# Performance work log

Hardware: AMD Instinct MI355X
Metric: run time of the kernel (lower is better)

Reference implementation:

```python
import jax, jax.numpy as jnp
import numpy as np

SEQ, D_IN, D_OUT, RANK, N_ADAPTERS = 8192, 4096, 4096, 16, 8


def setup_inputs() -> dict:
    key = jax.random.key(0)
    ks = jax.random.split(key, 7)
    return {
        "x": jax.random.normal(ks[0], (SEQ, D_IN), jnp.float32),
        "weight": jax.random.normal(ks[1], (D_IN, D_OUT), jnp.float32) * (D_IN ** -0.5),
        "bias": jax.random.normal(ks[2], (D_OUT,), jnp.float32),
        "A_buffer": jax.random.normal(ks[3], (N_ADAPTERS, RANK, D_IN), jnp.float32) * (D_IN ** -0.5),
        "B_buffer": jax.random.normal(ks[4], (N_ADAPTERS, D_OUT, RANK), jnp.float32) * (RANK ** -0.5),
        "scalings": jax.random.uniform(ks[5], (SEQ,), jnp.float32, 0.5, 2.0),
        "token_indices": jax.random.randint(ks[6], (SEQ,), 0, N_ADAPTERS, jnp.int32),
    }


def reference(x, weight, bias, A_buffer, B_buffer, scalings, token_indices):
    # Base linear layer: [S, D_in] @ [D_in, D_out] + bias
    base_output = x @ weight + bias
    n_adapters = A_buffer.shape[0]
    delta = jnp.zeros_like(base_output)
    # Grouped LoRA GEMM: per-adapter small GEMMs, masked scatter back per token.
    for e in range(n_adapters):
        # run_lora_a_gemm: x @ A[e]^T with per-token scaling -> [S, rank]
        a_out = (x @ A_buffer[e].T) * scalings[:, None]
        # run_lora_b_gemm: a_out @ B[e]^T -> [S, D_out]
        b_out = a_out @ B_buffer[e].T
        delta = delta + jnp.where((token_indices == e)[:, None], b_out, 0.0)
    return base_output + delta
```

## Files before the change

### kernel.cpp

```cpp
#include <hip/hip_runtime.h>
#include <hip/hip_bf16.h>
#include <cstdint>

#define SEQ   8192
#define DIN   4096
#define DOUT  4096
#define RANK  16
#define NAD   8
#define KC    (DIN + NAD*RANK)

using f32x4  = __attribute__((ext_vector_type(4))) float;
using bf16x8 = __attribute__((ext_vector_type(8))) short;

__device__ __forceinline__ unsigned short f2bf(float f) {
  union { float f; uint32_t u; } v; v.f = f;
  return (unsigned short)((v.u + 0x7fffu + ((v.u >> 16) & 1u)) >> 16);
}

__device__ __forceinline__ void async_copy16(void* lds, const void* gmem) {
  __builtin_amdgcn_global_load_lds(
      (__attribute__((address_space(1))) void*)(uintptr_t)gmem,
      (__attribute__((address_space(3))) void*)(uint32_t)(uintptr_t)lds,
      16, 0, 0);
}


__global__ void cvt_xa_kernel(const float* __restrict__ x, unsigned short* __restrict__ xcat,
                              const float* __restrict__ a, unsigned short* __restrict__ abf) {
  if (blockIdx.x < 4096) {
    const int64_t nchunks = (int64_t)SEQ * DIN / 8;
    for (int64_t c = (int64_t)blockIdx.x * 256 + threadIdx.x; c < nchunks;
         c += (int64_t)4096 * 256) {
      int64_t base = c * 8;
      int s = (int)(base >> 12);
      int k = (int)(base & (DIN - 1));
      float4 p = *(const float4*)(x + base);
      float4 q = *(const float4*)(x + base + 4);
      union { unsigned short h[8]; int4 v; } o;
      o.h[0]=f2bf(p.x); o.h[1]=f2bf(p.y); o.h[2]=f2bf(p.z); o.h[3]=f2bf(p.w);
      o.h[4]=f2bf(q.x); o.h[5]=f2bf(q.y); o.h[6]=f2bf(q.z); o.h[7]=f2bf(q.w);
      *(int4*)(xcat + (int64_t)s * KC + k) = o.v;
    }
  } else {
    int c = (blockIdx.x - 4096) * 256 + threadIdx.x;
    int64_t base = (int64_t)c * 8;
    float4 p = *(const float4*)(a + base);
    float4 q = *(const float4*)(a + base + 4);
    union { unsigned short h[8]; int4 v; } o;
    o.h[0]=f2bf(p.x); o.h[1]=f2bf(p.y); o.h[2]=f2bf(p.z); o.h[3]=f2bf(p.w);
    o.h[4]=f2bf(q.x); o.h[5]=f2bf(q.y); o.h[6]=f2bf(q.z); o.h[7]=f2bf(q.w);
    *(int4*)(abf + base) = o.v;
  }
}

__global__ void cvt_wb_kernel(const float* __restrict__ w, unsigned short* __restrict__ wcat,
                              const float* __restrict__ Bbuf) {
  if (blockIdx.x < 4096) {
    __shared__ unsigned short tls[64 * 68];
    int tt = threadIdx.x;
    int n0 = (blockIdx.x & 63) * 64;
    int k0 = (blockIdx.x >> 6) * 64;
#pragma unroll
    for (int j = 0; j < 8; j++) {
      int idx = j * 256 + tt;
      int kk = (idx >> 6) * 2;
      int nn = idx & 63;
      unsigned int lo = f2bf(w[(int64_t)(k0 + kk)     * DOUT + n0 + nn]);
      unsigned int hi = f2bf(w[(int64_t)(k0 + kk + 1) * DOUT + n0 + nn]);
      *(unsigned int*)&tls[nn * 68 + kk] = lo | (hi << 16);
    }
    __syncthreads();
#pragma unroll
    for (int pp = 0; pp < 4; pp++) {
      int flat = pp * 256 + tt;
      int nn = flat >> 4;
      int kk4 = (flat & 15) * 4;
      uint2 v = *(const uint2*)&tls[nn * 68 + kk4];
      *(uint2*)(wcat + (int64_t)(n0 + nn) * KC + k0 + kk4) = v;
    }
  } else {
    int idx = (blockIdx.x - 4096) * 256 + threadIdx.x;
    int n = idx >> 7, er = idx & 127;
    int e = er >> 4, r = er & 15;
    float v = Bbuf[((int64_t)e * DOUT + n) * RANK + r];
    wcat[(int64_t)n * KC + DIN + er] = f2bf(v);
  }
}

__global__ __launch_bounds__(512, 2) void gemm_lora_a2(
    const unsigned short* __restrict__ A,
    const unsigned short* __restrict__ Bb,
    const float* __restrict__ scal,
    const int* __restrict__ tok,
    unsigned short* __restrict__ xcat) {
  constexpr int BK = 64;
  __shared__ unsigned short sA[2][32 * BK];
  __shared__ unsigned short sB[2][128 * BK];
  int tid = threadIdx.x, wave = tid >> 6, lane = tid & 63;
  int quad = lane >> 4, l16 = lane & 15;
  int rm = wave >> 2, cn = wave & 3;
  int row0 = blockIdx.x * 32;
  int f8 = l16 & 7;

  f32x4 acc[2];
  acc[0] = f32x4{0.f, 0.f, 0.f, 0.f};
  acc[1] = f32x4{0.f, 0.f, 0.f, 0.f};

  auto stage = [&](int b, int kt) {
    int k0 = kt * BK;
    if (tid < 256) {
      int r = tid >> 3, kc = ((tid & 7) ^ (r & 7)) * 8;
      async_copy16(&sA[b][tid * 8], A + (int64_t)(row0 + r) * KC + k0 + kc);
    }
#pragma unroll
    for (int i = 0; i < 2; i++) {
      int c = i * 512 + tid;
      int r = c >> 3, kc = ((c & 7) ^ (r & 7)) * 8;
      async_copy16(&sB[b][c * 8], Bb + (int64_t)r * DIN + k0 + kc);
    }
  };

  stage(0, 0);
  __syncthreads();

  for (int kt = 0; kt < DIN / BK; ++kt) {
    int cur = kt & 1;
    if (kt + 1 < DIN / BK) stage(cur ^ 1, kt + 1);
    const unsigned short* sAc = sA[cur];
    const unsigned short* sBc = sB[cur];
#pragma unroll
    for (int ks = 0; ks < 2; ks++) {
      int qp = ((ks * 4 + quad) ^ f8) * 8;
      bf16x8 af = *(const bf16x8*)&sAc[(rm * 16 + l16) * BK + qp];
      bf16x8 b0 = *(const bf16x8*)&sBc[(cn * 32 + l16) * BK + qp];
      bf16x8 b1 = *(const bf16x8*)&sBc[(cn * 32 + 16 + l16) * BK + qp];
      acc[0] = __builtin_amdgcn_mfma_f32_16x16x32_bf16(af, b0, acc[0], 0, 0, 0);
      acc[1] = __builtin_amdgcn_mfma_f32_16x16x32_bf16(af, b1, acc[1], 0, 0, 0);
    }
    __syncthreads();
  }

#pragma unroll
  for (int ni = 0; ni < 2; ni++) {
    int er = cn * 32 + ni * 16 + l16;
    int e = er >> 4;
#pragma unroll
    for (int r = 0; r < 4; r++) {
      int s = row0 + rm * 16 + quad * 4 + r;
      float v = acc[ni][r] * scal[s];
      v = (e == tok[s]) ? v : 0.0f;
      xcat[(int64_t)s * KC + DIN + er] = f2bf(v);
    }
  }
}


#define CFENCE asm volatile("" ::: "memory")

template<int MQ>
__device__ __forceinline__ void ldsA(const unsigned short* aT, int wm, int l16, int quad,
                                     bf16x8 (&af)[4][2]) {
  int f8 = l16 & 7;
#pragma unroll
  for (int ks = 0; ks < 2; ks++) {
    int qp = ((ks * 4 + quad) ^ f8) * 8;
#pragma unroll
    for (int mi = 0; mi < 4; mi++)
      af[mi][ks] = *(const bf16x8*)&aT[(wm * 128 + MQ * 64 + mi * 16 + l16) * 64 + qp];
  }
}

template<int NQ>
__device__ __forceinline__ void ldsB(const unsigned short* bT, int wn, int l16, int quad,
                                     bf16x8 (&bq)[2][2]) {
  int f8 = l16 & 7;
#pragma unroll
  for (int ks = 0; ks < 2; ks++) {
    int qp = ((ks * 4 + quad) ^ f8) * 8;
#pragma unroll
    for (int ni = 0; ni < 2; ni++)
      bq[ni][ks] = *(const bf16x8*)&bT[(wn * 64 + NQ * 32 + ni * 16 + l16) * 64 + qp];
  }
}

template<int MQ, int NQ>
__device__ __forceinline__ void mfma_quad(f32x4 (&acc)[8][4], bf16x8 (&af)[4][2],
                                          bf16x8 (&bq)[2][2]) {
  __builtin_amdgcn_s_setprio(1);
#pragma unroll
  for (int mi = 0; mi < 4; mi++)
#pragma unroll
    for (int ni = 0; ni < 2; ni++)
#pragma unroll
      for (int ks = 0; ks < 2; ks++)
        acc[MQ * 4 + mi][NQ * 2 + ni] = __builtin_amdgcn_mfma_f32_16x16x32_bf16(
            af[mi][ks], bq[ni][ks], acc[MQ * 4 + mi][NQ * 2 + ni], 0, 0, 0);
  __builtin_amdgcn_s_setprio(0);
}

__device__ __forceinline__ void stage_A(unsigned short* sAb, const unsigned short* Ag,
                                        int mq, int k0, int tid) {
  int rr  = tid >> 3;
  int q8  = (tid & 7) * 8;
  int qc8 = ((tid & 7) ^ (rr & 7)) * 8;
  int r0 = mq * 64 + rr;
  async_copy16(sAb + r0 * 64 + q8, Ag + (int64_t)r0 * KC + k0 + qc8);
  int r1 = r0 + 128;
  async_copy16(sAb + r1 * 64 + q8, Ag + (int64_t)r1 * KC + k0 + qc8);
}

__device__ __forceinline__ void stage_B(unsigned short* sBb, const unsigned short* Bg,
                                        int nq, int k0, int tid) {
  int rB  = ((tid >> 3) & 31) | ((tid >> 8) << 6);
  int q8  = (tid & 7) * 8;
  int qc8 = ((tid & 7) ^ ((tid >> 3) & 7)) * 8;
  int r0 = nq * 32 + rB;
  async_copy16(sBb + r0 * 64 + q8, Bg + (int64_t)r0 * KC + k0 + qc8);
  int r1 = r0 + 128;
  async_copy16(sBb + r1 * 64 + q8, Bg + (int64_t)r1 * KC + k0 + qc8);
}

#define MIDBAR                                                    \
  CFENCE; __builtin_amdgcn_s_barrier();                           \
  asm volatile("s_waitcnt lgkmcnt(0)" ::: "memory")
#define ENDBAR  CFENCE; __builtin_amdgcn_s_barrier(); CFENCE

#define TILE(aT, bT, S0, S1, S2, S3, BND)                         \
  ldsA<0>(aT, wm, l16, quad, af);                                 \
  ldsB<0>(bT, wn, l16, quad, bf0);                                \
  S0; MIDBAR;                                                     \
  mfma_quad<0, 0>(acc, af, bf0);                                  \
  ENDBAR;                                                         \
  ldsB<1>(bT, wn, l16, quad, bf1);                                \
  S1; MIDBAR;                                                     \
  mfma_quad<0, 1>(acc, af, bf1);                                  \
  ENDBAR;                                                         \
  ldsA<1>(aT, wm, l16, quad, af);                                 \
  S2; MIDBAR;                                                     \
  mfma_quad<1, 1>(acc, af, bf1);                                  \
  ENDBAR;                                                         \
  S3; CFENCE;                                                     \
  mfma_quad<1, 0>(acc, af, bf0);                                  \
  BND;                                                            \
  ENDBAR

__global__ __launch_bounds__(512, 2) void gemm_main8(
    const unsigned short* __restrict__ A,
    const unsigned short* __restrict__ B,
    const float* __restrict__ bias,
    float* __restrict__ out) {
  extern __shared__ unsigned short smem[];
  unsigned short* a0 = smem;
  unsigned short* b0 = smem + 16384;
  unsigned short* a1 = smem + 32768;
  unsigned short* b1 = smem + 49152;

  int tid = threadIdx.x, wave = tid >> 6, lane = tid & 63;
  int quad = lane >> 4, l16 = lane & 15;
  int wm = wave >> 2, wn = wave & 3;

  int bid = blockIdx.x;
  int cid = (bid & 7) * 64 + (bid >> 3);
  int bm = cid >> 4, bn = cid & 15;
  int row0 = bm * 256, col0 = bn * 256;

  const unsigned short* Ag = A + (int64_t)row0 * KC;
  const unsigned short* Bg = B + (int64_t)col0 * KC;

  const f32x4 zero = {0.f, 0.f, 0.f, 0.f};
  f32x4 acc[8][4];
#pragma unroll
  for (int i = 0; i < 8; i++)
#pragma unroll
    for (int j = 0; j < 4; j++) acc[i][j] = zero;

  bf16x8 af[4][2], bf0[2][2], bf1[2][2];

  stage_A(a0, Ag, 0, 0, tid);
  stage_B(b0, Bg, 0, 0, tid);
  stage_B(b0, Bg, 1, 0, tid);
  stage_A(a0, Ag, 1, 0, tid);
  stage_A(a1, Ag, 0, 64, tid);
  stage_B(b1, Bg, 1, 64, tid);
  stage_A(a1, Ag, 1, 64, tid);
  asm volatile("s_waitcnt vmcnt(6)" ::: "memory");
  ENDBAR;

#define BND6 asm volatile("s_waitcnt vmcnt(6)" ::: "memory")

  for (int tp = 0; tp < 32; ++tp) {
    int kE = tp * 128;
    TILE(a0, b0,
         stage_B(b1, Bg, 0, kE + 64,  tid),
         stage_A(a0, Ag, 0, kE + 128, tid),
         stage_B(b0, Bg, 1, kE + 128, tid),
         stage_A(a0, Ag, 1, kE + 128, tid),
         BND6);
    TILE(a1, b1,
         stage_B(b0, Bg, 0, kE + 128, tid),
         stage_A(a1, Ag, 0, kE + 192, tid),
         stage_B(b1, Bg, 1, kE + 192, tid),
         stage_A(a1, Ag, 1, kE + 192, tid),
         BND6);
  }

  TILE(a0, b0,
       stage_B(b1, Bg, 0, 4160, tid),
       (void)0, (void)0, (void)0,
       asm volatile("s_waitcnt vmcnt(0)" ::: "memory"));

  ldsA<0>(a1, wm, l16, quad, af);
  ldsB<0>(b1, wn, l16, quad, bf0);
  mfma_quad<0, 0>(acc, af, bf0);
  ldsB<1>(b1, wn, l16, quad, bf1);
  mfma_quad<0, 1>(acc, af, bf1);
  ldsA<1>(a1, wm, l16, quad, af);
  mfma_quad<1, 1>(acc, af, bf1);
  mfma_quad<1, 0>(acc, af, bf0);

#pragma unroll
  for (int ni = 0; ni < 4; ni++) {
    int col = col0 + wn * 64 + ni * 16 + l16;
    float bv = bias[col];
#pragma unroll
    for (int mi = 0; mi < 8; mi++) {
      int rbase = row0 + wm * 128 + mi * 16 + quad * 4;
#pragma unroll
      for (int r = 0; r < 4; r++)
        out[(int64_t)(rbase + r) * DOUT + col] = acc[mi][ni][r] + bv;
    }
  }
}

__global__ void fb_aout(const float* __restrict__ x, const float* __restrict__ Abuf,
                        const float* __restrict__ scal, const int* __restrict__ tok,
                        float* __restrict__ aout) {
  int s = blockIdx.x;
  int e = tok[s];
  __shared__ float red[256];
  for (int r = 0; r < RANK; ++r) {
    float p = 0.f;
    for (int k = threadIdx.x; k < DIN; k += 256)
      p += x[(int64_t)s * DIN + k] * Abuf[((int64_t)e * RANK + r) * DIN + k];
    red[threadIdx.x] = p;
    __syncthreads();
    for (int off = 128; off > 0; off >>= 1) {
      if (threadIdx.x < off) red[threadIdx.x] += red[threadIdx.x + off];
      __syncthreads();
    }
    if (threadIdx.x == 0) aout[s * RANK + r] = red[0] * scal[s];
    __syncthreads();
  }
}
__global__ void fb_out(const float* __restrict__ x, const float* __restrict__ w,
                       const float* __restrict__ bias, const float* __restrict__ Bbuf,
                       const int* __restrict__ tok, const float* __restrict__ aout,
                       float* __restrict__ out) {
  int64_t idx = (int64_t)blockIdx.x * blockDim.x + threadIdx.x;
  int s = (int)(idx >> 12), n = (int)(idx & (DOUT - 1));
  float accv = bias[n];
  for (int k = 0; k < DIN; ++k)
    accv += x[(int64_t)s * DIN + k] * w[(int64_t)k * DOUT + n];
  int e = tok[s];
  float d = 0.f;
  for (int r = 0; r < RANK; ++r)
    d += aout[s * RANK + r] * Bbuf[((int64_t)e * DOUT + n) * RANK + r];
  out[idx] = accv + d;
}

extern "C" void kernel_launch(void* const* d_in, const int* in_sizes, int n_in,
                              void* d_out, int out_size, void* d_ws, size_t ws_size,
                              hipStream_t stream) {
  const float* x    = (const float*)d_in[0];
  const float* w    = (const float*)d_in[1];
  const float* bias = (const float*)d_in[2];
  const float* Abuf = (const float*)d_in[3];
  const float* Bbuf = (const float*)d_in[4];
  const float* scal = (const float*)d_in[5];
  const int*   tok  = (const int*)d_in[6];
  float* out = (float*)d_out;

  const size_t xcat_b = (size_t)SEQ * KC * 2;
  const size_t wcat_b = (size_t)DOUT * KC * 2;
  const size_t abf_b  = (size_t)NAD * RANK * DIN * 2;

  if (ws_size >= xcat_b + wcat_b + abf_b) {
    static bool lds_attr_done = false;
    if (!lds_attr_done) {
      (void)hipFuncSetAttribute((const void*)gemm_main8,
                                hipFuncAttributeMaxDynamicSharedMemorySize, 131072);
      lds_attr_done = true;
    }
    unsigned short* xcat = (unsigned short*)d_ws;
    unsigned short* wcat = (unsigned short*)((char*)d_ws + xcat_b);
    unsigned short* abf  = (unsigned short*)((char*)d_ws + xcat_b + wcat_b);
    cvt_xa_kernel<<<4352, 256, 0, stream>>>(x, xcat, Abuf, abf);
    cvt_wb_kernel<<<6144, 256, 0, stream>>>(w, wcat, Bbuf);
    gemm_lora_a2<<<256, 512, 0, stream>>>(xcat, abf, scal, tok, xcat);
    gemm_main8<<<512, 512, 131072, stream>>>(xcat, wcat, bias, out);
  } else {
    float* aout = (float*)d_ws;
    fb_aout<<<SEQ, 256, 0, stream>>>(x, Abuf, scal, tok, aout);
    fb_out<<<(int)(((int64_t)SEQ * DOUT) / 256), 256, 0, stream>>>(x, w, bias, Bbuf, tok, aout, out);
  }
}
```

Measured before the change: 552.5 us.

## Fuse x bf16 conversion into LoRA-A GEMM and merge weight/A conversion kernels

The LoRA-A GEMM now reads fp32 x directly, converts each tile to bf16 in registers, writes it into the swizzled LDS tile and also stores it into xcat for the main GEMM. This removes the separate x conversion pass and the re-read of bf16 x from global memory. W/B and A conversions are merged into one launch, saving a kernel launch. In exchange, the LoRA-A kernel uses synchronous global loads for x, which adds register pressure and latency per K step, and it drops the 2-blocks-per-CU launch bound hint. Only 256 blocks now do the x conversion work, so that work is less parallel than before.

```diff
diff --git a/kernel.cpp b/kernel.cpp
--- a/kernel.cpp
+++ b/kernel.cpp
@@ -24,25 +24,40 @@
       16, 0, 0);
 }
 
-
-__global__ void cvt_xa_kernel(const float* __restrict__ x, unsigned short* __restrict__ xcat,
-                              const float* __restrict__ a, unsigned short* __restrict__ abf) {
+__global__ void cvt_wba_kernel(const float* __restrict__ w, unsigned short* __restrict__ wcat,
+                               const float* __restrict__ Bbuf,
+                               const float* __restrict__ a, unsigned short* __restrict__ abf) {
   if (blockIdx.x < 4096) {
-    const int64_t nchunks = (int64_t)SEQ * DIN / 8;
-    for (int64_t c = (int64_t)blockIdx.x * 256 + threadIdx.x; c < nchunks;
-         c += (int64_t)4096 * 256) {
-      int64_t base = c * 8;
-      int s = (int)(base >> 12);
-      int k = (int)(base & (DIN - 1));
-      float4 p = *(const float4*)(x + base);
-      float4 q = *(const float4*)(x + base + 4);
-      union { unsigned short h[8]; int4 v; } o;
-      o.h[0]=f2bf(p.x); o.h[1]=f2bf(p.y); o.h[2]=f2bf(p.z); o.h[3]=f2bf(p.w);
-      o.h[4]=f2bf(q.x); o.h[5]=f2bf(q.y); o.h[6]=f2bf(q.z); o.h[7]=f2bf(q.w);
-      *(int4*)(xcat + (int64_t)s * KC + k) = o.v;
-    }
+    __shared__ unsigned short tls[64 * 68];
+    int tt = threadIdx.x;
+    int n0 = (blockIdx.x & 63) * 64;
+    int k0 = (blockIdx.x >> 6) * 64;
+#pragma unroll
+    for (int j = 0; j < 8; j++) {
+      int idx = j * 256 + tt;
+      int kk = (idx >> 6) * 2;
+      int nn = idx & 63;
+      unsigned int lo = f2bf(w[(int64_t)(k0 + kk)     * DOUT + n0 + nn]);
+      unsigned int hi = f2bf(w[(int64_t)(k0 + kk + 1) * DOUT + n0 + nn]);
+      *(unsigned int*)&tls[nn * 68 + kk] = lo | (hi << 16);
+    }
+    __syncthreads();
+#pragma unroll
+    for (int pp = 0; pp < 4; pp++) {
+      int flat = pp * 256 + tt;
+      int nn = flat >> 4;
+      int kk4 = (flat & 15) * 4;
+      uint2 v = *(const uint2*)&tls[nn * 68 + kk4];
+      *(uint2*)(wcat + (int64_t)(n0 + nn) * KC + k0 + kk4) = v;
+    }
+  } else if (blockIdx.x < 6144) {
+    int idx = (blockIdx.x - 4096) * 256 + threadIdx.x;
+    int n = idx >> 7, er = idx & 127;
+    int e = er >> 4, r = er & 15;
+    float v = Bbuf[((int64_t)e * DOUT + n) * RANK + r];
+    wcat[(int64_t)n * KC + DIN + er] = f2bf(v);
   } else {
-    int c = (blockIdx.x - 4096) * 256 + threadIdx.x;
+    int c = (blockIdx.x - 6144) * 256 + threadIdx.x;
     int64_t base = (int64_t)c * 8;
     float4 p = *(const float4*)(a + base);
     float4 q = *(const float4*)(a + base + 4);
@@ -53,42 +68,8 @@
   }
 }
 
-__global__ void cvt_wb_kernel(const float* __restrict__ w, unsigned short* __restrict__ wcat,
-                              const float* __restrict__ Bbuf) {
-  if (blockIdx.x < 4096) {
-    __shared__ unsigned short tls[64 * 68];
-    int tt = threadIdx.x;
-    int n0 = (blockIdx.x & 63) * 64;
-    int k0 = (blockIdx.x >> 6) * 64;
-#pragma unroll
-    for (int j = 0; j < 8; j++) {
-      int idx = j * 256 + tt;
-      int kk = (idx >> 6) * 2;
-      int nn = idx & 63;
-      unsigned int lo = f2bf(w[(int64_t)(k0 + kk)     * DOUT + n0 + nn]);
-      unsigned int hi = f2bf(w[(int64_t)(k0 + kk + 1) * DOUT + n0 + nn]);
-      *(unsigned int*)&tls[nn * 68 + kk] = lo | (hi << 16);
-    }
-    __syncthreads();
-#pragma unroll
-    for (int pp = 0; pp < 4; pp++) {
-      int flat = pp * 256 + tt;
-      int nn = flat >> 4;
-      int kk4 = (flat & 15) * 4;
-      uint2 v = *(const uint2*)&tls[nn * 68 + kk4];
-      *(uint2*)(wcat + (int64_t)(n0 + nn) * KC + k0 + kk4) = v;
-    }
-  } else {
-    int idx = (blockIdx.x - 4096) * 256 + threadIdx.x;
-    int n = idx >> 7, er = idx & 127;
-    int e = er >> 4, r = er & 15;
-    float v = Bbuf[((int64_t)e * DOUT + n) * RANK + r];
-    wcat[(int64_t)n * KC + DIN + er] = f2bf(v);
-  }
-}
-
-__global__ __launch_bounds__(512, 2) void gemm_lora_a2(
-    const unsigned short* __restrict__ A,
+__global__ __launch_bounds__(512) void xlora_kernel(
+    const float* __restrict__ x,
     const unsigned short* __restrict__ Bb,
     const float* __restrict__ scal,
     const int* __restrict__ tok,
@@ -102,16 +83,19 @@
   int row0 = blockIdx.x * 32;
   int f8 = l16 & 7;
 
+  int xr = tid >> 4, c4 = (tid & 15) * 4;
+  int qi = c4 >> 3;
+  int qsw = ((qi ^ (xr & 7)) * 8) + (c4 & 7);
+
+  const float* xp = x + (int64_t)(row0 + xr) * DIN + c4;
+  unsigned short* xcp = xcat + (int64_t)(row0 + xr) * KC + c4;
+
   f32x4 acc[2];
   acc[0] = f32x4{0.f, 0.f, 0.f, 0.f};
   acc[1] = f32x4{0.f, 0.f, 0.f, 0.f};
 
-  auto stage = [&](int b, int kt) {
+  auto stageB = [&](int b, int kt) {
     int k0 = kt * BK;
-    if (tid < 256) {
-      int r = tid >> 3, kc = ((tid & 7) ^ (r & 7)) * 8;
-      async_copy16(&sA[b][tid * 8], A + (int64_t)(row0 + r) * KC + k0 + kc);
-    }
 #pragma unroll
     for (int i = 0; i < 2; i++) {
       int c = i * 512 + tid;
@@ -120,12 +104,24 @@
     }
   };
 
-  stage(0, 0);
+  {
+    float4 xv = *(const float4*)xp;
+    stageB(0, 0);
+    union { unsigned short h[4]; uint2 v; } o;
+    o.h[0]=f2bf(xv.x); o.h[1]=f2bf(xv.y); o.h[2]=f2bf(xv.z); o.h[3]=f2bf(xv.w);
+    *(uint2*)&sA[0][xr * BK + qsw] = o.v;
+    *(uint2*)xcp = o.v;
+  }
   __syncthreads();
 
   for (int kt = 0; kt < DIN / BK; ++kt) {
     int cur = kt & 1;
-    if (kt + 1 < DIN / BK) stage(cur ^ 1, kt + 1);
+    bool hasNext = (kt + 1 < DIN / BK);
+    float4 xn;
+    if (hasNext) {
+      xn = *(const float4*)(xp + (kt + 1) * BK);
+      stageB(cur ^ 1, kt + 1);
+    }
     const unsigned short* sAc = sA[cur];
     const unsigned short* sBc = sB[cur];
 #pragma unroll
@@ -136,6 +132,12 @@
       bf16x8 b1 = *(const bf16x8*)&sBc[(cn * 32 + 16 + l16) * BK + qp];
       acc[0] = __builtin_amdgcn_mfma_f32_16x16x32_bf16(af, b0, acc[0], 0, 0, 0);
       acc[1] = __builtin_amdgcn_mfma_f32_16x16x32_bf16(af, b1, acc[1], 0, 0, 0);
+    }
+    if (hasNext) {
+      union { unsigned short h[4]; uint2 v; } on;
+      on.h[0]=f2bf(xn.x); on.h[1]=f2bf(xn.y); on.h[2]=f2bf(xn.z); on.h[3]=f2bf(xn.w);
+      *(uint2*)&sA[cur ^ 1][xr * BK + qsw] = on.v;
+      *(uint2*)(xcp + (kt + 1) * BK) = on.v;
     }
     __syncthreads();
   }
@@ -394,9 +396,8 @@
     unsigned short* xcat = (unsigned short*)d_ws;
     unsigned short* wcat = (unsigned short*)((char*)d_ws + xcat_b);
     unsigned short* abf  = (unsigned short*)((char*)d_ws + xcat_b + wcat_b);
-    cvt_xa_kernel<<<4352, 256, 0, stream>>>(x, xcat, Abuf, abf);
-    cvt_wb_kernel<<<6144, 256, 0, stream>>>(w, wcat, Bbuf);
-    gemm_lora_a2<<<256, 512, 0, stream>>>(xcat, abf, scal, tok, xcat);
+    cvt_wba_kernel<<<6400, 256, 0, stream>>>(w, wcat, Bbuf, Abuf, abf);
+    xlora_kernel<<<256, 512, 0, stream>>>(x, abf, scal, tok, xcat);
     gemm_main8<<<512, 512, 131072, stream>>>(xcat, wcat, bias, out);
   } else {
     float* aout = (float*)d_ws;
```

New measurement: 521.5 us. 1.06x faster.
